# Kernel optimization log

Measured on AMD Instinct MI355X. Metric: run time of the kernel, lower is better.

Reference implementation:

```python
import jax, jax.numpy as jnp
import numpy as np

BSZ = 32768
K = 4096  # 1 positive + (K-1) negatives

def setup_inputs() -> dict:
    key = jax.random.key(0)
    x = jax.random.normal(key, (BSZ, K), dtype=jnp.float32)
    # ~mean CE for random logits is log(K)~8.3 -> mask keeps roughly half the samples
    threshold = jnp.float32(8.3)
    return {"x": x, "threshold": threshold}

def reference(x, threshold):
    # per-sample cross-entropy vs label 0: -log_softmax(x)[:, 0]
    loss = jax.nn.logsumexp(x, axis=1) - x[:, 0]          # [BSZ]
    mask = (loss > threshold).astype(loss.dtype)          # [BSZ]
    count = mask.sum()
    loss_t = (loss * mask).sum()
    # if no element exceeds threshold: count=1, loss_t=loss[0]
    return jnp.where(count == 0, loss[0], loss_t / jnp.maximum(count, 1.0))
```

## Files before the change

kernel.cpp:

```cpp
#include <hip/hip_runtime.h>
#include <math.h>

#define K_DIM 4096
#define BSZ 32768
#define BLOCK 256
#define WAVES (BLOCK / 64)

__global__ __launch_bounds__(BLOCK) void row_loss_kernel(
    const float* __restrict__ x, float* __restrict__ loss_out) {
  __shared__ float s_red[WAVES];

  const int row = blockIdx.x;
  const int t = threadIdx.x;
  const float4* xr = reinterpret_cast<const float4*>(x) + (size_t)row * (K_DIM / 4);

  float4 v[4];
#pragma unroll
  for (int i = 0; i < 4; ++i) v[i] = xr[i * BLOCK + t];

  const float x0 = v[0].x;

  float m = v[0].x;
#pragma unroll
  for (int i = 0; i < 4; ++i) {
    m = fmaxf(m, fmaxf(fmaxf(v[i].x, v[i].y), fmaxf(v[i].z, v[i].w)));
  }
#pragma unroll
  for (int off = 32; off >= 1; off >>= 1) m = fmaxf(m, __shfl_xor(m, off));

  const int wave = t >> 6;
  const int lane = t & 63;
  if (lane == 0) s_red[wave] = m;
  __syncthreads();
  const float rowmax =
      fmaxf(fmaxf(s_red[0], s_red[1]), fmaxf(s_red[2], s_red[3]));
  __syncthreads();

  float s = 0.f;
#pragma unroll
  for (int i = 0; i < 4; ++i) {
    s += __expf(v[i].x - rowmax);
    s += __expf(v[i].y - rowmax);
    s += __expf(v[i].z - rowmax);
    s += __expf(v[i].w - rowmax);
  }
#pragma unroll
  for (int off = 32; off >= 1; off >>= 1) s += __shfl_xor(s, off);
  if (lane == 0) s_red[wave] = s;
  __syncthreads();

  if (t == 0) {
    float total = s_red[0] + s_red[1] + s_red[2] + s_red[3];
    loss_out[row] = rowmax + __logf(total) - x0;
  }
}

__global__ __launch_bounds__(1024) void finalize_kernel(
    const float* __restrict__ loss, const float* __restrict__ thr_p,
    float* __restrict__ out) {
  __shared__ float s_sum[1024 / 64];
  __shared__ float s_cnt[1024 / 64];

  const float thr = *thr_p;
  const int t = threadIdx.x;

  float sum = 0.f, cnt = 0.f;
  for (int i = t; i < BSZ; i += 1024) {
    float l = loss[i];
    if (l > thr) {
      sum += l;
      cnt += 1.f;
    }
  }
#pragma unroll
  for (int off = 32; off >= 1; off >>= 1) {
    sum += __shfl_xor(sum, off);
    cnt += __shfl_xor(cnt, off);
  }
  const int wave = t >> 6;
  const int lane = t & 63;
  if (lane == 0) {
    s_sum[wave] = sum;
    s_cnt[wave] = cnt;
  }
  __syncthreads();
  if (t == 0) {
    float S = 0.f, C = 0.f;
#pragma unroll
    for (int w = 0; w < 1024 / 64; ++w) {
      S += s_sum[w];
      C += s_cnt[w];
    }
    out[0] = (C == 0.f) ? loss[0] : S / fmaxf(C, 1.f);
  }
}

extern "C" void kernel_launch(void* const* d_in, const int* in_sizes, int n_in,
                              void* d_out, int out_size, void* d_ws,
                              size_t ws_size, hipStream_t stream) {
  const float* x = (const float*)d_in[0];
  const float* thr = (const float*)d_in[1];
  float* out = (float*)d_out;
  float* loss = (float*)d_ws;

  row_loss_kernel<<<BSZ, BLOCK, 0, stream>>>(x, loss);
  finalize_kernel<<<1, 1024, 0, stream>>>(loss, thr, out);
}
```

Before: 102.1 us.

## Map one wave per row, drop block barriers, use nontemporal loads

Each 64-lane wave now handles four rows in sequence and keeps a full 4096-element row in registers as 16 float4 per lane. The reduction uses only wave shuffles, so the shared-memory staging and __syncthreads are gone, and the grid shrinks to 2048 blocks. Loads of x use nontemporal hints and the finalize kernel reads losses as float4. The costs are higher register pressure, which may lower occupancy, and less memory-level parallelism per row, since each row's loads are issued only when that row starts.

```diff
diff --git a/kernel.cpp b/kernel.cpp
--- a/kernel.cpp
+++ b/kernel.cpp
@@ -4,54 +4,51 @@
 #define K_DIM 4096
 #define BSZ 32768
 #define BLOCK 256
-#define WAVES (BLOCK / 64)
+#define WAVES_PER_BLOCK (BLOCK / 64)
+#define ROWS_PER_WAVE 4
+#define GRID (BSZ / (WAVES_PER_BLOCK * ROWS_PER_WAVE))
+
+typedef float f32x4 __attribute__((ext_vector_type(4)));
 
 __global__ __launch_bounds__(BLOCK) void row_loss_kernel(
     const float* __restrict__ x, float* __restrict__ loss_out) {
-  __shared__ float s_red[WAVES];
+  const int t = threadIdx.x;
+  const int lane = t & 63;
+  const int gw = blockIdx.x * WAVES_PER_BLOCK + (t >> 6);
 
-  const int row = blockIdx.x;
-  const int t = threadIdx.x;
-  const float4* xr = reinterpret_cast<const float4*>(x) + (size_t)row * (K_DIM / 4);
+  const f32x4* x4 = reinterpret_cast<const f32x4*>(x);
 
-  float4 v[4];
 #pragma unroll
-  for (int i = 0; i < 4; ++i) v[i] = xr[i * BLOCK + t];
+  for (int r = 0; r < ROWS_PER_WAVE; ++r) {
+    const int row = gw * ROWS_PER_WAVE + r;
+    const f32x4* xr = x4 + (size_t)row * (K_DIM / 4);
 
-  const float x0 = v[0].x;
+    f32x4 v[16];
+#pragma unroll
+    for (int i = 0; i < 16; ++i) {
+      v[i] = __builtin_nontemporal_load(xr + i * 64 + lane);
+    }
 
-  float m = v[0].x;
+    const float x0 = v[0].x;
+
+    float m = v[0].x;
 #pragma unroll
-  for (int i = 0; i < 4; ++i) {
-    m = fmaxf(m, fmaxf(fmaxf(v[i].x, v[i].y), fmaxf(v[i].z, v[i].w)));
-  }
+    for (int i = 0; i < 16; ++i) {
+      m = fmaxf(m, fmaxf(fmaxf(v[i].x, v[i].y), fmaxf(v[i].z, v[i].w)));
+    }
 #pragma unroll
-  for (int off = 32; off >= 1; off >>= 1) m = fmaxf(m, __shfl_xor(m, off));
+    for (int off = 32; off >= 1; off >>= 1) m = fmaxf(m, __shfl_xor(m, off));
 
-  const int wave = t >> 6;
-  const int lane = t & 63;
-  if (lane == 0) s_red[wave] = m;
-  __syncthreads();
-  const float rowmax =
-      fmaxf(fmaxf(s_red[0], s_red[1]), fmaxf(s_red[2], s_red[3]));
-  __syncthreads();
+    float s = 0.f;
+#pragma unroll
+    for (int i = 0; i < 16; ++i) {
+      s += __expf(v[i].x - m) + __expf(v[i].y - m) + __expf(v[i].z - m) +
+           __expf(v[i].w - m);
+    }
+#pragma unroll
+    for (int off = 32; off >= 1; off >>= 1) s += __shfl_xor(s, off);
 
-  float s = 0.f;
-#pragma unroll
-  for (int i = 0; i < 4; ++i) {
-    s += __expf(v[i].x - rowmax);
-    s += __expf(v[i].y - rowmax);
-    s += __expf(v[i].z - rowmax);
-    s += __expf(v[i].w - rowmax);
-  }
-#pragma unroll
-  for (int off = 32; off >= 1; off >>= 1) s += __shfl_xor(s, off);
-  if (lane == 0) s_red[wave] = s;
-  __syncthreads();
-
-  if (t == 0) {
-    float total = s_red[0] + s_red[1] + s_red[2] + s_red[3];
-    loss_out[row] = rowmax + __logf(total) - x0;
+    if (lane == 0) loss_out[row] = m + __logf(s) - x0;
   }
 }
 
@@ -63,13 +60,19 @@
 
   const float thr = *thr_p;
   const int t = threadIdx.x;
+  const f32x4* l4 = reinterpret_cast<const f32x4*>(loss);
 
   float sum = 0.f, cnt = 0.f;
-  for (int i = t; i < BSZ; i += 1024) {
-    float l = loss[i];
-    if (l > thr) {
-      sum += l;
-      cnt += 1.f;
+#pragma unroll
+  for (int i = 0; i < BSZ / 4 / 1024; ++i) {
+    f32x4 v = l4[i * 1024 + t];
+#pragma unroll
+    for (int j = 0; j < 4; ++j) {
+      float l = v[j];
+      if (l > thr) {
+        sum += l;
+        cnt += 1.f;
+      }
     }
   }
 #pragma unroll
@@ -103,6 +106,6 @@
   float* out = (float*)d_out;
   float* loss = (float*)d_ws;
 
-  row_loss_kernel<<<BSZ, BLOCK, 0, stream>>>(x, loss);
+  row_loss_kernel<<<GRID, BLOCK, 0, stream>>>(x, loss);
   finalize_kernel<<<1, 1024, 0, stream>>>(loss, thr, out);
 }
```

Result: faster. 93.11 us (-8.8%).
